# Optimization experiments

Measured on AMD Instinct MI355X. Metric: run time of the kernel, lower is better.

Reference implementation:

```python
import jax, jax.numpy as jnp
import numpy as np
from jax import lax

EPS = 1e-10

def _safe_norm(x):
    # torch remove_zeros: replace exact-zero norms with 1e-10
    n = jnp.linalg.norm(x, axis=-1, keepdims=True)
    return jnp.where(n != 0, n, jnp.full_like(n, EPS))

def setup_inputs() -> dict:
    key = jax.random.key(0)
    ks = jax.random.split(key, 5)
    S, B, D = 2048, 32, 512  # seq, batch, 2*hidden
    K = 147  # odd(max_entries/14)
    return {
        "encoder_outputs": jax.random.normal(ks[0], (S, B, D), dtype=jnp.float32),
        "state": jax.random.normal(ks[1], (B, D), dtype=jnp.float32),
        "previous_attention": jax.random.uniform(ks[2], (B, S), dtype=jnp.float32),
        "W_att": jax.random.normal(ks[3], (D, D), dtype=jnp.float32) / np.sqrt(D),
        "b_att": jax.random.normal(ks[4], (D,), dtype=jnp.float32) * 0.01,
        "conv_w": jnp.ones((1, 1, K), dtype=jnp.float32),
        "conv_b": jnp.zeros((1,), dtype=jnp.float32),
    }

def reference(encoder_outputs, state, previous_attention, W_att, b_att, conv_w, conv_b):
    S, B, D = encoder_outputs.shape
    # attended state via linear layer, then cosine-similarity weights (vectorized over seq)
    attended = state @ W_att.T + b_att                       # [B, D]
    ns = attended / _safe_norm(attended)                     # [B, D]
    ne = encoder_outputs / _safe_norm(encoder_outputs)       # [S, B, D]
    weights = jnp.einsum('bd,sbd->bs', ns, ne)               # [B, S]
    # conv1d time smoothing of previous attention (same-length, odd kernel)
    k = conv_w.shape[-1]
    pad = k // 2
    y = lax.conv_general_dilated(previous_attention[:, None, :], conv_w,
                                 window_strides=(1,), padding=[(pad, pad)])
    adjusted = jax.nn.relu(y[:, 0, :] + conv_b)              # [B, S]
    prev_probs = adjusted / jnp.sum(adjusted, axis=1, keepdims=True)
    adj = prev_probs * jax.nn.softmax(weights, axis=1)
    norm_w = adj / jnp.sum(adj, axis=1, keepdims=True)       # [B, S]
    applied = jnp.einsum('bs,sbd->bd', norm_w, encoder_outputs)  # [B, D]
    return applied, norm_w
```

## Files before the change

### kernel.cpp

```cpp
#include <hip/hip_runtime.h>
#include <hip/hip_bf16.h>
#include <math.h>


__device__ __forceinline__ float wave_sum(float v) {
    for (int off = 32; off; off >>= 1) v += __shfl_xor(v, off);
    return v;
}
__device__ __forceinline__ float wave_max(float v) {
    for (int off = 32; off; off >>= 1) v = fmaxf(v, __shfl_xor(v, off));
    return v;
}

__global__ __launch_bounds__(128) void linear_kernel(
    const float* __restrict__ state, const float* __restrict__ W,
    const float* __restrict__ bias, float* __restrict__ attended, int D) {
    int b = blockIdx.y;
    int d = blockIdx.x * 128 + threadIdx.x;
    __shared__ __align__(16) float st[512];
    ((float4*)st)[threadIdx.x] = ((const float4*)(state + (size_t)b * D))[threadIdx.x];
    __syncthreads();

    const float4* Wrow = (const float4*)(W + (size_t)d * D);
    const float4* sv = (const float4*)st;
    float acc = bias[d];
#pragma unroll 8
    for (int k = 0; k < 128; ++k) {
        float4 w = Wrow[k];
        float4 s4 = sv[k];
        acc += w.x * s4.x + w.y * s4.y + w.z * s4.z + w.w * s4.w;
    }
    attended[(size_t)b * D + d] = acc;
}

__global__ __launch_bounds__(512) void rownorm_kernel(
    const float* __restrict__ attended, float* __restrict__ ns, int D) {
    int b = blockIdx.x;
    int d = threadIdx.x;
    float v = attended[(size_t)b * D + d];
    float sq = wave_sum(v * v);
    __shared__ float red[8];
    int lane = d & 63, wv = d >> 6;
    if (lane == 0) red[wv] = sq;
    __syncthreads();
    float t = red[0] + red[1] + red[2] + red[3] + red[4] + red[5] + red[6] + red[7];
    float n = sqrtf(t);
    if (n == 0.f) n = 1e-10f;
    ns[(size_t)b * D + d] = v / n;
}

__global__ __launch_bounds__(256) void conv_relu_kernel(
    const float* __restrict__ prev, const float* __restrict__ cw,
    const float* __restrict__ cb, float* __restrict__ adj, int S, int K) {
    int b = blockIdx.y;
    int s0 = blockIdx.x * 256;
    int t = threadIdx.x;
    int pad = K / 2;
    __shared__ float seg[256 + 192];
    __shared__ float wk[192];
    int seglen = 256 + K - 1;
    for (int i = t; i < seglen; i += 256) {
        int s = s0 - pad + i;
        seg[i] = (s >= 0 && s < S) ? prev[(size_t)b * S + s] : 0.f;
    }
    for (int j = t; j < K; j += 256) wk[j] = cw[j];
    __syncthreads();

    float y = cb[0];
    for (int j = 0; j < K; ++j) y += seg[t + j] * wk[j];
    adj[(size_t)b * S + s0 + t] = fmaxf(y, 0.f);
}

__global__ __launch_bounds__(256) void cos_weights_kernel(
    const float* __restrict__ e, const float* __restrict__ ns,
    float* __restrict__ weights, int S, int B, int D) {
    int wid = (blockIdx.x * 256 + threadIdx.x) >> 6;
    int lane = threadIdx.x & 63;
    int b = wid % B;
    int s = wid / B;
    const float4* ev = (const float4*)(e + ((size_t)s * B + b) * D);
    const float4* nv = (const float4*)(ns + (size_t)b * D);
    float dot = 0.f, sq = 0.f;
#pragma unroll
    for (int k = 0; k < 2; ++k) {
        float4 x = ev[lane + 64 * k];
        float4 y = nv[lane + 64 * k];
        dot += x.x * y.x + x.y * y.y + x.z * y.z + x.w * y.w;
        sq  += x.x * x.x + x.y * x.y + x.z * x.z + x.w * x.w;
    }
    dot = wave_sum(dot);
    sq = wave_sum(sq);
    if (lane == 0) {
        float n = sqrtf(sq);
        if (n == 0.f) n = 1e-10f;
        weights[(size_t)b * S + s] = dot / n;
    }
}

__global__ __launch_bounds__(256) void softmax_combine_kernel(
    const float* __restrict__ weights, const float* __restrict__ adj,
    float* __restrict__ norm_w, int S) {
    int b = blockIdx.x;
    int t = threadIdx.x;
    int lane = t & 63, wv = t >> 6;
    __shared__ float red[4];
    const float* wrow = weights + (size_t)b * S;
    const float* arow = adj + (size_t)b * S;

    float m = -INFINITY;
    for (int s = t; s < S; s += 256) m = fmaxf(m, wrow[s]);
    m = wave_max(m);
    if (lane == 0) red[wv] = m;
    __syncthreads();
    m = fmaxf(fmaxf(red[0], red[1]), fmaxf(red[2], red[3]));
    __syncthreads();

    float lsum = 0.f;
    for (int s = t; s < S; s += 256) lsum += arow[s] * expf(wrow[s] - m);
    lsum = wave_sum(lsum);
    if (lane == 0) red[wv] = lsum;
    __syncthreads();
    float Z = red[0] + red[1] + red[2] + red[3];
    float inv = 1.f / Z;
    for (int s = t; s < S; s += 256)
        norm_w[(size_t)b * S + s] = arow[s] * expf(wrow[s] - m) * inv;
}

__global__ __launch_bounds__(128) void apply_partial_kernel(
    const float* __restrict__ e, const float* __restrict__ nw,
    float* __restrict__ partial, int S, int B, int D, int CH) {
    int b = blockIdx.y;
    int c = blockIdx.x;
    int s0 = c * CH;
    int t = threadIdx.x;
    float4 acc = {0.f, 0.f, 0.f, 0.f};
    for (int s = s0; s < s0 + CH; ++s) {
        float wgt = nw[(size_t)b * S + s];
        float4 x = ((const float4*)(e + ((size_t)s * B + b) * D))[t];
        acc.x += wgt * x.x;
        acc.y += wgt * x.y;
        acc.z += wgt * x.z;
        acc.w += wgt * x.w;
    }
    ((float4*)(partial + ((size_t)c * B + b) * D))[t] = acc;
}

__global__ __launch_bounds__(128) void apply_reduce_kernel(
    const float* __restrict__ partial, float* __restrict__ applied,
    int B, int D, int NC) {
    int b = blockIdx.x;
    int t = threadIdx.x;
    float4 acc = {0.f, 0.f, 0.f, 0.f};
    for (int c = 0; c < NC; ++c) {
        float4 x = ((const float4*)(partial + ((size_t)c * B + b) * D))[t];
        acc.x += x.x; acc.y += x.y; acc.z += x.z; acc.w += x.w;
    }
    ((float4*)(applied + (size_t)b * D))[t] = acc;
}

extern "C" void kernel_launch(void* const* d_in, const int* in_sizes, int n_in,
                              void* d_out, int out_size, void* d_ws, size_t ws_size,
                              hipStream_t stream) {
    const float* enc   = (const float*)d_in[0];
    const float* state = (const float*)d_in[1];
    const float* prev  = (const float*)d_in[2];
    const float* W     = (const float*)d_in[3];
    const float* bias  = (const float*)d_in[4];
    const float* cw    = (const float*)d_in[5];
    const float* cb    = (const float*)d_in[6];

    const int S = in_sizes[0] / in_sizes[1];
    const int B = in_sizes[2] / S;
    const int D = in_sizes[1] / B;
    const int K = in_sizes[5];

    float* out     = (float*)d_out;
    float* applied = out;
    float* norm_w  = out + (size_t)B * D;

    const int NC = 32;
    const int CH = S / NC;

    float* ws       = (float*)d_ws;
    float* attended = ws;
    float* ns       = attended + (size_t)B * D;
    float* adj      = ns + (size_t)B * D;
    float* weights  = adj + (size_t)B * S;
    float* partial  = weights + (size_t)B * S;

    linear_kernel<<<dim3(D / 128, B), 128, 0, stream>>>(state, W, bias, attended, D);
    conv_relu_kernel<<<dim3(S / 256, B), 256, 0, stream>>>(prev, cw, cb, adj, S, K);
    rownorm_kernel<<<B, D, 0, stream>>>(attended, ns, D);
    cos_weights_kernel<<<(S * B) / 4, 256, 0, stream>>>(enc, ns, weights, S, B, D);
    softmax_combine_kernel<<<B, 256, 0, stream>>>(weights, adj, norm_w, S);
    apply_partial_kernel<<<dim3(NC, B), 128, 0, stream>>>(enc, norm_w, partial, S, B, D, CH);
    apply_reduce_kernel<<<B, 128, 0, stream>>>(partial, applied, B, D, NC);
}
```

Before: 254.6 us.

## Fuse cosine weights, softmax and weighted sum into single-pass encoder kernel

Merges the linear layer and conv smoothing into one launch, and folds the row normalisation, cosine-weight computation, exp weighting and weighted accumulation into one kernel. That kernel reads each encoder row once and emits partial sums plus per-chunk normalisers. The max-subtraction in the softmax is dropped, which is safe only because cosine similarities are bounded in [-1,1]. The change removes the second full pass over the 134 MB encoder tensor and several launches, at the cost of a serial per-row wave reduction inside the streaming loop.

```diff
diff --git a/kernel.cpp b/kernel.cpp
--- a/kernel.cpp
+++ b/kernel.cpp
@@ -7,155 +7,146 @@
     for (int off = 32; off; off >>= 1) v += __shfl_xor(v, off);
     return v;
 }
-__device__ __forceinline__ float wave_max(float v) {
-    for (int off = 32; off; off >>= 1) v = fmaxf(v, __shfl_xor(v, off));
-    return v;
-}
 
-__global__ __launch_bounds__(128) void linear_kernel(
+__global__ __launch_bounds__(256) void front_kernel(
     const float* __restrict__ state, const float* __restrict__ W,
-    const float* __restrict__ bias, float* __restrict__ attended, int D) {
+    const float* __restrict__ bias, const float* __restrict__ prev,
+    const float* __restrict__ cw, const float* __restrict__ cb,
+    float* __restrict__ attended, float* __restrict__ adj,
+    int S, int D, int K) {
+    __shared__ __align__(16) float smem[1024];
     int b = blockIdx.y;
-    int d = blockIdx.x * 128 + threadIdx.x;
-    __shared__ __align__(16) float st[512];
-    ((float4*)st)[threadIdx.x] = ((const float4*)(state + (size_t)b * D))[threadIdx.x];
-    __syncthreads();
+    int t = threadIdx.x;
 
-    const float4* Wrow = (const float4*)(W + (size_t)d * D);
-    const float4* sv = (const float4*)st;
-    float acc = bias[d];
+    if (blockIdx.x < 2) {
+        if (t < D / 4)
+            ((float4*)smem)[t] = ((const float4*)(state + (size_t)b * D))[t];
+        __syncthreads();
+        int d = blockIdx.x * 256 + t;
+        const float4* Wrow = (const float4*)(W + (size_t)d * D);
+        const float4* sv = (const float4*)smem;
+        float acc = bias[d];
 #pragma unroll 8
-    for (int k = 0; k < 128; ++k) {
-        float4 w = Wrow[k];
-        float4 s4 = sv[k];
-        acc += w.x * s4.x + w.y * s4.y + w.z * s4.z + w.w * s4.w;
-    }
-    attended[(size_t)b * D + d] = acc;
-}
-
-__global__ __launch_bounds__(512) void rownorm_kernel(
-    const float* __restrict__ attended, float* __restrict__ ns, int D) {
-    int b = blockIdx.x;
-    int d = threadIdx.x;
-    float v = attended[(size_t)b * D + d];
-    float sq = wave_sum(v * v);
-    __shared__ float red[8];
-    int lane = d & 63, wv = d >> 6;
-    if (lane == 0) red[wv] = sq;
-    __syncthreads();
-    float t = red[0] + red[1] + red[2] + red[3] + red[4] + red[5] + red[6] + red[7];
-    float n = sqrtf(t);
-    if (n == 0.f) n = 1e-10f;
-    ns[(size_t)b * D + d] = v / n;
-}
-
-__global__ __launch_bounds__(256) void conv_relu_kernel(
-    const float* __restrict__ prev, const float* __restrict__ cw,
-    const float* __restrict__ cb, float* __restrict__ adj, int S, int K) {
-    int b = blockIdx.y;
-    int s0 = blockIdx.x * 256;
-    int t = threadIdx.x;
-    int pad = K / 2;
-    __shared__ float seg[256 + 192];
-    __shared__ float wk[192];
-    int seglen = 256 + K - 1;
-    for (int i = t; i < seglen; i += 256) {
-        int s = s0 - pad + i;
-        seg[i] = (s >= 0 && s < S) ? prev[(size_t)b * S + s] : 0.f;
-    }
-    for (int j = t; j < K; j += 256) wk[j] = cw[j];
-    __syncthreads();
-
-    float y = cb[0];
-    for (int j = 0; j < K; ++j) y += seg[t + j] * wk[j];
-    adj[(size_t)b * S + s0 + t] = fmaxf(y, 0.f);
-}
-
-__global__ __launch_bounds__(256) void cos_weights_kernel(
-    const float* __restrict__ e, const float* __restrict__ ns,
-    float* __restrict__ weights, int S, int B, int D) {
-    int wid = (blockIdx.x * 256 + threadIdx.x) >> 6;
-    int lane = threadIdx.x & 63;
-    int b = wid % B;
-    int s = wid / B;
-    const float4* ev = (const float4*)(e + ((size_t)s * B + b) * D);
-    const float4* nv = (const float4*)(ns + (size_t)b * D);
-    float dot = 0.f, sq = 0.f;
-#pragma unroll
-    for (int k = 0; k < 2; ++k) {
-        float4 x = ev[lane + 64 * k];
-        float4 y = nv[lane + 64 * k];
-        dot += x.x * y.x + x.y * y.y + x.z * y.z + x.w * y.w;
-        sq  += x.x * x.x + x.y * x.y + x.z * x.z + x.w * x.w;
-    }
-    dot = wave_sum(dot);
-    sq = wave_sum(sq);
-    if (lane == 0) {
-        float n = sqrtf(sq);
-        if (n == 0.f) n = 1e-10f;
-        weights[(size_t)b * S + s] = dot / n;
+        for (int k = 0; k < 128; ++k) {
+            float4 w4 = Wrow[k];
+            float4 s4 = sv[k];
+            acc += w4.x * s4.x + w4.y * s4.y + w4.z * s4.z + w4.w * s4.w;
+        }
+        attended[(size_t)b * D + d] = acc;
+    } else {
+        int s0 = (blockIdx.x - 2) * 256;
+        int pad = K / 2;
+        int seglen = 256 + K - 1;
+        float* seg = smem;
+        float* wk = smem + 512;
+        for (int i = t; i < seglen; i += 256) {
+            int s = s0 - pad + i;
+            seg[i] = (s >= 0 && s < S) ? prev[(size_t)b * S + s] : 0.f;
+        }
+        for (int j = t; j < K; j += 256) wk[j] = cw[j];
+        __syncthreads();
+        float y = cb[0];
+        for (int j = 0; j < K; ++j) y += seg[t + j] * wk[j];
+        adj[(size_t)b * S + s0 + t] = fmaxf(y, 0.f);
     }
 }
 
-__global__ __launch_bounds__(256) void softmax_combine_kernel(
-    const float* __restrict__ weights, const float* __restrict__ adj,
-    float* __restrict__ norm_w, int S) {
+__global__ __launch_bounds__(256) void main_kernel(
+    const float* __restrict__ e, const float* __restrict__ attended,
+    const float* __restrict__ adj, float* __restrict__ partial,
+    float* __restrict__ zbuf, float* __restrict__ u,
+    int S, int B, int D, int CH) {
+    int wave = threadIdx.x >> 6;
+    int lane = threadIdx.x & 63;
+    int c = blockIdx.x * 4 + wave;
+    int b = blockIdx.y;
+
+    const float4* att4 = (const float4*)(attended + (size_t)b * D);
+    float4 a0 = att4[lane];
+    float4 a1 = att4[lane + 64];
+    float asq = a0.x * a0.x + a0.y * a0.y + a0.z * a0.z + a0.w * a0.w
+              + a1.x * a1.x + a1.y * a1.y + a1.z * a1.z + a1.w * a1.w;
+    asq = wave_sum(asq);
+    float an = sqrtf(asq);
+    if (an == 0.f) an = 1e-10f;
+    float ainv = 1.f / an;
+    float4 ns0, ns1;
+    ns0.x = a0.x * ainv; ns0.y = a0.y * ainv; ns0.z = a0.z * ainv; ns0.w = a0.w * ainv;
+    ns1.x = a1.x * ainv; ns1.y = a1.y * ainv; ns1.z = a1.z * ainv; ns1.w = a1.w * ainv;
+
+    float4 acc0 = {0.f, 0.f, 0.f, 0.f};
+    float4 acc1 = {0.f, 0.f, 0.f, 0.f};
+    float z = 0.f;
+
+    int s0 = c * CH;
+    const float4* row4 = (const float4*)(e + ((size_t)s0 * B + b) * D);
+    size_t rstride = (size_t)B * D / 4;
+
+    float4 x0 = row4[lane];
+    float4 x1 = row4[lane + 64];
+    for (int i = 0; i < CH; ++i) {
+        float4 nx0, nx1;
+        if (i + 1 < CH) {
+            nx0 = row4[rstride + lane];
+            nx1 = row4[rstride + lane + 64];
+        }
+        float dot = x0.x * ns0.x + x0.y * ns0.y + x0.z * ns0.z + x0.w * ns0.w
+                  + x1.x * ns1.x + x1.y * ns1.y + x1.z * ns1.z + x1.w * ns1.w;
+        float sq  = x0.x * x0.x + x0.y * x0.y + x0.z * x0.z + x0.w * x0.w
+                  + x1.x * x1.x + x1.y * x1.y + x1.z * x1.z + x1.w * x1.w;
+        dot = wave_sum(dot);
+        sq  = wave_sum(sq);
+        float n = sqrtf(sq);
+        if (n == 0.f) n = 1e-10f;
+        float w = dot / n;
+        float coef = adj[(size_t)b * S + s0 + i] * __expf(w);
+        if (lane == 0) u[(size_t)b * S + s0 + i] = coef;
+        acc0.x += coef * x0.x; acc0.y += coef * x0.y;
+        acc0.z += coef * x0.z; acc0.w += coef * x0.w;
+        acc1.x += coef * x1.x; acc1.y += coef * x1.y;
+        acc1.z += coef * x1.z; acc1.w += coef * x1.w;
+        z += coef;
+        x0 = nx0; x1 = nx1;
+        row4 += rstride;
+    }
+
+    float4* p4 = (float4*)(partial + ((size_t)c * B + b) * D);
+    p4[lane] = acc0;
+    p4[lane + 64] = acc1;
+    if (lane == 0) zbuf[(size_t)c * B + b] = z;
+}
+
+__global__ __launch_bounds__(256) void combine_kernel(
+    const float* __restrict__ partial, const float* __restrict__ zbuf,
+    const float* __restrict__ u, float* __restrict__ applied,
+    float* __restrict__ norm_w, int S, int B, int D, int NCB) {
     int b = blockIdx.x;
     int t = threadIdx.x;
     int lane = t & 63, wv = t >> 6;
     __shared__ float red[4];
-    const float* wrow = weights + (size_t)b * S;
-    const float* arow = adj + (size_t)b * S;
+    __shared__ float zsh;
 
-    float m = -INFINITY;
-    for (int s = t; s < S; s += 256) m = fmaxf(m, wrow[s]);
-    m = wave_max(m);
-    if (lane == 0) red[wv] = m;
+    float zt = (t < NCB) ? zbuf[(size_t)t * B + b] : 0.f;
+    zt = wave_sum(zt);
+    if (lane == 0) red[wv] = zt;
     __syncthreads();
-    m = fmaxf(fmaxf(red[0], red[1]), fmaxf(red[2], red[3]));
+    if (t == 0) zsh = 1.f / (red[0] + red[1] + red[2] + red[3]);
     __syncthreads();
+    float inv = zsh;
 
-    float lsum = 0.f;
-    for (int s = t; s < S; s += 256) lsum += arow[s] * expf(wrow[s] - m);
-    lsum = wave_sum(lsum);
-    if (lane == 0) red[wv] = lsum;
-    __syncthreads();
-    float Z = red[0] + red[1] + red[2] + red[3];
-    float inv = 1.f / Z;
+    if (t < D / 4) {
+        float4 acc = {0.f, 0.f, 0.f, 0.f};
+        const float4* p4 = (const float4*)partial;
+        for (int c = 0; c < NCB; ++c) {
+            float4 x = p4[((size_t)c * B + b) * (D / 4) + t];
+            acc.x += x.x; acc.y += x.y; acc.z += x.z; acc.w += x.w;
+        }
+        acc.x *= inv; acc.y *= inv; acc.z *= inv; acc.w *= inv;
+        ((float4*)(applied + (size_t)b * D))[t] = acc;
+    }
+
     for (int s = t; s < S; s += 256)
-        norm_w[(size_t)b * S + s] = arow[s] * expf(wrow[s] - m) * inv;
-}
-
-__global__ __launch_bounds__(128) void apply_partial_kernel(
-    const float* __restrict__ e, const float* __restrict__ nw,
-    float* __restrict__ partial, int S, int B, int D, int CH) {
-    int b = blockIdx.y;
-    int c = blockIdx.x;
-    int s0 = c * CH;
-    int t = threadIdx.x;
-    float4 acc = {0.f, 0.f, 0.f, 0.f};
-    for (int s = s0; s < s0 + CH; ++s) {
-        float wgt = nw[(size_t)b * S + s];
-        float4 x = ((const float4*)(e + ((size_t)s * B + b) * D))[t];
-        acc.x += wgt * x.x;
-        acc.y += wgt * x.y;
-        acc.z += wgt * x.z;
-        acc.w += wgt * x.w;
-    }
-    ((float4*)(partial + ((size_t)c * B + b) * D))[t] = acc;
-}
-
-__global__ __launch_bounds__(128) void apply_reduce_kernel(
-    const float* __restrict__ partial, float* __restrict__ applied,
-    int B, int D, int NC) {
-    int b = blockIdx.x;
-    int t = threadIdx.x;
-    float4 acc = {0.f, 0.f, 0.f, 0.f};
-    for (int c = 0; c < NC; ++c) {
-        float4 x = ((const float4*)(partial + ((size_t)c * B + b) * D))[t];
-        acc.x += x.x; acc.y += x.y; acc.z += x.z; acc.w += x.w;
-    }
-    ((float4*)(applied + (size_t)b * D))[t] = acc;
+        norm_w[(size_t)b * S + s] = u[(size_t)b * S + s] * inv;
 }
 
 extern "C" void kernel_launch(void* const* d_in, const int* in_sizes, int n_in,
@@ -178,21 +169,20 @@
     float* applied = out;
     float* norm_w  = out + (size_t)B * D;
 
-    const int NC = 32;
-    const int CH = S / NC;
+    const int NCB = 128;
+    const int CH = S / NCB;
 
     float* ws       = (float*)d_ws;
     float* attended = ws;
-    float* ns       = attended + (size_t)B * D;
-    float* adj      = ns + (size_t)B * D;
-    float* weights  = adj + (size_t)B * S;
-    float* partial  = weights + (size_t)B * S;
+    float* adj      = attended + (size_t)B * D;
+    float* u        = adj + (size_t)B * S;
+    float* zbuf     = u + (size_t)B * S;
+    float* partial  = zbuf + (size_t)NCB * B;
 
-    linear_kernel<<<dim3(D / 128, B), 128, 0, stream>>>(state, W, bias, attended, D);
-    conv_relu_kernel<<<dim3(S / 256, B), 256, 0, stream>>>(prev, cw, cb, adj, S, K);
-    rownorm_kernel<<<B, D, 0, stream>>>(attended, ns, D);
-    cos_weights_kernel<<<(S * B) / 4, 256, 0, stream>>>(enc, ns, weights, S, B, D);
-    softmax_combine_kernel<<<B, 256, 0, stream>>>(weights, adj, norm_w, S);
-    apply_partial_kernel<<<dim3(NC, B), 128, 0, stream>>>(enc, norm_w, partial, S, B, D, CH);
-    apply_reduce_kernel<<<B, 128, 0, stream>>>(partial, applied, B, D, NC);
+    front_kernel<<<dim3(2 + S / 256, B), 256, 0, stream>>>(
+        state, W, bias, prev, cw, cb, attended, adj, S, D, K);
+    main_kernel<<<dim3(NCB / 4, B), 256, 0, stream>>>(
+        enc, attended, adj, partial, zbuf, u, S, B, D, CH);
+    combine_kernel<<<B, 256, 0, stream>>>(
+        partial, zbuf, u, applied, norm_w, S, B, D, NCB);
 }
```

Result: no change. 252.3 us (-0.9%).
